# Kernel tuning notes

Measured on AMD Instinct MI355X. Metric: run time of the kernel, lower is better.

## Reference

```python
import jax, jax.numpy as jnp
import numpy as np
from jax.ops import segment_sum

N_NODES = 50000
N_EDGES = 150000
IN_FEATS = 512
OUT_FEATS = 512


def setup_inputs() -> dict:
    key = jax.random.key(0)
    k1, k2, k3, k4 = jax.random.split(key, 4)
    x = jax.random.normal(k1, (N_NODES, IN_FEATS), dtype=jnp.float32)
    src = jax.random.randint(k2, (N_EDGES,), 0, N_NODES, dtype=jnp.int64)
    dst = jax.random.randint(k3, (N_EDGES,), 0, N_NODES, dtype=jnp.int64)
    # Xavier-uniform init like reset_parameters
    limit = float(np.sqrt(6.0 / (IN_FEATS + OUT_FEATS)))
    W = jax.random.uniform(k4, (IN_FEATS, OUT_FEATS), dtype=jnp.float32,
                           minval=-limit, maxval=limit)
    b = jnp.zeros((OUT_FEATS,), dtype=jnp.float32)
    return {"x": x, "src": src, "dst": dst, "W": W, "b": b}


def reference(x, src, dst, W, b):
    # DGL GraphConv with norm='both':
    #   out = relu( D_dst^{-1/2} A D_src^{-1/2} X W + b )
    # Dropout is identity in eval mode (training=False).
    ones = jnp.ones((src.shape[0],), dtype=x.dtype)
    deg_out = segment_sum(ones, src, num_segments=N_NODES)  # source out-degree
    deg_in = segment_sum(ones, dst, num_segments=N_NODES)   # dest in-degree
    norm_src = jnp.where(deg_out > 0, deg_out, 1.0) ** -0.5  # [N]
    norm_dst = jnp.where(deg_in > 0, deg_in, 1.0) ** -0.5    # [N]

    h = x * norm_src[:, None]                         # [N, in]
    agg = segment_sum(h[src], dst, num_segments=N_NODES)  # scatter-add over edges
    agg = agg * norm_dst[:, None]                     # [N, in]
    out = agg @ W + b                                 # [N, out]
    return jax.nn.relu(out)
```

## Files before the change

### kernel.cpp

```cpp
#include <hip/hip_runtime.h>
#include <hip/hip_bf16.h>

#define N_NODES 50000
#define N_PAD   50048
#define N_EDGES 150000
#define F 512
#define BM 128
#define BN 128
#define BK 64
#define NBLK 196

typedef __attribute__((ext_vector_type(4))) float f32x4;
typedef __attribute__((ext_vector_type(4))) unsigned int u32x4;
typedef __attribute__((ext_vector_type(2))) unsigned int u32x2;

__device__ __forceinline__ unsigned short f2bf(float f) {
    unsigned int u = __float_as_uint(f);
    return (unsigned short)((u + 0x7fffu + ((u >> 16) & 1u)) >> 16);
}
__device__ __forceinline__ unsigned int pack2(float a, float b) {
    return (unsigned int)f2bf(a) | ((unsigned int)f2bf(b) << 16);
}
__device__ __forceinline__ void gload16(const void* g, void* l) {
    __builtin_amdgcn_global_load_lds(
        (const __attribute__((address_space(1))) unsigned int*)g,
        (__attribute__((address_space(3))) unsigned int*)l, 16, 0, 0);
}

__global__ void __launch_bounds__(256) crd_deg(const int* __restrict__ src,
                                               const int* __restrict__ dst,
                                               int* __restrict__ hist) {
    int e = blockIdx.x * 256 + threadIdx.x;
    if (e < N_EDGES) {
        atomicAdd(&hist[src[e]], 1);
        atomicAdd(&hist[N_NODES + dst[e]], 1);
    }
}

__global__ void __launch_bounds__(256) crd_norm(const int* __restrict__ hist,
                                                float* __restrict__ norms) {
    int i = blockIdx.x * 256 + threadIdx.x;
    if (i < 2 * N_NODES) {
        int d = hist[i];
        norms[i] = rsqrtf((float)(d > 0 ? d : 1));
    }
}

__global__ void __launch_bounds__(256) crd_bsum(const int* __restrict__ hist_in,
                                                int* __restrict__ bsum) {
    __shared__ int s[256];
    int t = threadIdx.x;
    int i = blockIdx.x * 256 + t;
    s[t] = (i < N_NODES) ? hist_in[i] : 0;
    __syncthreads();
    #pragma unroll
    for (int o = 128; o > 0; o >>= 1) {
        if (t < o) s[t] += s[t + o];
        __syncthreads();
    }
    if (t == 0) bsum[blockIdx.x] = s[0];
}

__global__ void __launch_bounds__(256) crd_bscan(const int* __restrict__ bsum,
                                                 int* __restrict__ bsumoff) {
    __shared__ int s[256];
    int t = threadIdx.x;
    int v = (t < NBLK) ? bsum[t] : 0;
    s[t] = v;
    __syncthreads();
    #pragma unroll
    for (int d = 1; d < 256; d <<= 1) {
        int add = (t >= d) ? s[t - d] : 0;
        __syncthreads();
        s[t] += add;
        __syncthreads();
    }
    if (t < NBLK) bsumoff[t] = s[t] - v;
}

__global__ void __launch_bounds__(256) crd_escan(const int* __restrict__ hist_in,
                                                 const int* __restrict__ bsumoff,
                                                 int* __restrict__ off,
                                                 int* __restrict__ cursor) {
    __shared__ int s[256];
    int t = threadIdx.x;
    int i = blockIdx.x * 256 + t;
    int v = (i < N_NODES) ? hist_in[i] : 0;
    s[t] = v;
    __syncthreads();
    #pragma unroll
    for (int d = 1; d < 256; d <<= 1) {
        int add = (t >= d) ? s[t - d] : 0;
        __syncthreads();
        s[t] += add;
        __syncthreads();
    }
    int excl = s[t] - v + bsumoff[blockIdx.x];
    if (i < N_NODES) { off[i] = excl; cursor[i] = excl; }
    if (i == N_NODES - 1) off[N_NODES] = excl + v;
}

__global__ void __launch_bounds__(256) crd_place(const int* __restrict__ src,
                                                 const int* __restrict__ dst,
                                                 int* __restrict__ cursor,
                                                 int* __restrict__ sorted) {
    int e = blockIdx.x * 256 + threadIdx.x;
    if (e < N_EDGES) {
        int slot = atomicAdd(&cursor[dst[e]], 1);
        sorted[slot] = src[e];
    }
}

__global__ void __launch_bounds__(256) crd_wt(const float* __restrict__ W,
                                              unsigned short* __restrict__ Wt) {
    int idx = blockIdx.x * 256 + threadIdx.x;
    int n = idx >> 9, k = idx & 511;
    Wt[idx] = f2bf(W[k * F + n]);
}

__global__ void __launch_bounds__(256) crd_xb(const float* __restrict__ x,
                                              unsigned short* __restrict__ xb) {
    size_t i = (size_t)(blockIdx.x * 256 + threadIdx.x) * 8;
    f32x4 v0 = *(const f32x4*)(x + i);
    f32x4 v1 = *(const f32x4*)(x + i + 4);
    u32x4 w;
    w.x = pack2(v0.x, v0.y); w.y = pack2(v0.z, v0.w);
    w.z = pack2(v1.x, v1.y); w.w = pack2(v1.z, v1.w);
    *(u32x4*)(xb + i) = w;
}

__global__ void __launch_bounds__(256) crd_gather_bf(const unsigned short* __restrict__ xb,
                                                     const int* __restrict__ sorted,
                                                     const int* __restrict__ off,
                                                     const float* __restrict__ norms,
                                                     unsigned short* __restrict__ aggb) {
    int wid = (blockIdx.x * 256 + threadIdx.x) >> 6;
    int lane = threadIdx.x & 63;
    if (wid >= N_PAD) return;
    float a0=0.f,a1=0.f,a2=0.f,a3=0.f,a4=0.f,a5=0.f,a6=0.f,a7=0.f;
    if (wid < N_NODES) {
        int e0 = off[wid], e1 = off[wid + 1];
        for (int e = e0; e < e1; ++e) {
            int s = sorted[e];
            float ns = norms[s];
            u32x4 v = *(const u32x4*)(xb + (size_t)s * F + lane * 8);
            a0 += __uint_as_float(v.x << 16) * ns;
            a1 += __uint_as_float(v.x & 0xffff0000u) * ns;
            a2 += __uint_as_float(v.y << 16) * ns;
            a3 += __uint_as_float(v.y & 0xffff0000u) * ns;
            a4 += __uint_as_float(v.z << 16) * ns;
            a5 += __uint_as_float(v.z & 0xffff0000u) * ns;
            a6 += __uint_as_float(v.w << 16) * ns;
            a7 += __uint_as_float(v.w & 0xffff0000u) * ns;
        }
        float nd = norms[N_NODES + wid];
        a0*=nd;a1*=nd;a2*=nd;a3*=nd;a4*=nd;a5*=nd;a6*=nd;a7*=nd;
    }
    u32x4 w;
    w.x = pack2(a0, a1); w.y = pack2(a2, a3);
    w.z = pack2(a4, a5); w.w = pack2(a6, a7);
    *(u32x4*)(aggb + (size_t)wid * F + lane * 8) = w;
}

__global__ void __launch_bounds__(256) crd_gather_f32(const float* __restrict__ x,
                                                      const int* __restrict__ sorted,
                                                      const int* __restrict__ off,
                                                      const float* __restrict__ norms,
                                                      unsigned short* __restrict__ aggb) {
    int wid = (blockIdx.x * 256 + threadIdx.x) >> 6;
    int lane = threadIdx.x & 63;
    if (wid >= N_PAD) return;
    f32x4 a0 = {0.f,0.f,0.f,0.f}, a1 = a0;
    if (wid < N_NODES) {
        int e0 = off[wid], e1 = off[wid + 1];
        for (int e = e0; e < e1; ++e) {
            int s = sorted[e];
            float ns = norms[s];
            const f32x4* p = (const f32x4*)(x + (size_t)s * F);
            a0 += p[lane] * ns;
            a1 += p[64 + lane] * ns;
        }
        float nd = norms[N_NODES + wid];
        a0 *= nd; a1 *= nd;
    }
    unsigned short* row = aggb + (size_t)wid * F;
    u32x2 w0, w1;
    w0.x = pack2(a0.x, a0.y); w0.y = pack2(a0.z, a0.w);
    w1.x = pack2(a1.x, a1.y); w1.y = pack2(a1.z, a1.w);
    *(u32x2*)(row + lane * 4) = w0;
    *(u32x2*)(row + 256 + lane * 4) = w1;
}

__global__ void __launch_bounds__(256, 3) crd_gemm(const unsigned short* __restrict__ aggb,
                                                   const unsigned short* __restrict__ Wt,
                                                   const float* __restrict__ bias,
                                                   float* __restrict__ out) {
    __shared__ __align__(16) unsigned short lA[8 * BM * 8];
    __shared__ __align__(16) unsigned short lB[8 * BN * 8];
    const int tid = threadIdx.x;
    const int rowbase = blockIdx.x * BM;
    const int nbase = blockIdx.y * BN;
    const int lane = tid & 63;
    const int wave = tid >> 6;
    const int wm = wave >> 1, wn = wave & 1;
    const int g = lane >> 4, r = lane & 15;

    f32x4 zero4 = {0.f, 0.f, 0.f, 0.f};
    f32x4 acc[4][4];
    #pragma unroll
    for (int i = 0; i < 4; ++i)
        #pragma unroll
        for (int j = 0; j < 4; ++j) acc[i][j] = zero4;

    for (int ks = 0; ks < F / BK; ++ks) {
        #pragma unroll
        for (int j = 0; j < 4; ++j) {
            int gg = (wave * 4 + j) * 64 + lane;
            int k8 = gg >> 7, row = gg & 127;
            gload16(aggb + (size_t)(rowbase + row) * F + ks * BK + k8 * 8,
                    &lA[(size_t)(wave * 4 + j) * 64 * 8]);
        }
        #pragma unroll
        for (int j = 0; j < 4; ++j) {
            int gg = (wave * 4 + j) * 64 + lane;
            int k8 = gg >> 7, n = gg & 127;
            gload16(Wt + (size_t)(nbase + n) * F + ks * BK + k8 * 8,
                    &lB[(size_t)(wave * 4 + j) * 64 * 8]);
        }
        __syncthreads();
        #pragma unroll
        for (int kk = 0; kk < 2; ++kk) {
            int k8 = kk * 4 + g;
            u32x4 af[4], bfr[4];
            #pragma unroll
            for (int mi = 0; mi < 4; ++mi)
                af[mi] = *(const u32x4*)&lA[(k8 * BM + wm * 64 + mi * 16 + r) * 8];
            #pragma unroll
            for (int ni = 0; ni < 4; ++ni)
                bfr[ni] = *(const u32x4*)&lB[(k8 * BN + wn * 64 + ni * 16 + r) * 8];
            #pragma unroll
            for (int mi = 0; mi < 4; ++mi)
                #pragma unroll
                for (int ni = 0; ni < 4; ++ni)
                    asm("v_mfma_f32_16x16x32_bf16 %0, %1, %2, %0"
                        : "+v"(acc[mi][ni])
                        : "v"(af[mi]), "v"(bfr[ni]));
        }
        __syncthreads();
    }
    #pragma unroll
    for (int ni = 0; ni < 4; ++ni) {
        int col = nbase + wn * 64 + ni * 16 + r;
        float bv = bias[col];
        #pragma unroll
        for (int mi = 0; mi < 4; ++mi) {
            #pragma unroll
            for (int j = 0; j < 4; ++j) {
                int row = rowbase + wm * 64 + mi * 16 + g * 4 + j;
                if (row < N_NODES) {
                    float v = acc[mi][ni][j] + bv;
                    out[(size_t)row * F + col] = v > 0.0f ? v : 0.0f;
                }
            }
        }
    }
}

extern "C" void kernel_launch(void* const* d_in, const int* in_sizes, int n_in,
                              void* d_out, int out_size, void* d_ws, size_t ws_size,
                              hipStream_t stream) {
    const float* x = (const float*)d_in[0];
    const int* src = (const int*)d_in[1];
    const int* dst = (const int*)d_in[2];
    const float* W = (const float*)d_in[3];
    const float* bias = (const float*)d_in[4];
    float* out = (float*)d_out;

    unsigned short* aggb = (unsigned short*)d_ws;
    unsigned short* Wt = aggb + (size_t)N_PAD * F;
    float* norms = (float*)(Wt + (size_t)F * F);
    int* hist = (int*)(norms + 2 * N_NODES);
    int* off = hist + 2 * N_NODES;
    int* cursor = off + N_NODES + 1;
    int* sorted = cursor + N_NODES;
    int* bsum = sorted + N_EDGES;
    int* bsumoff = bsum + NBLK;
    char* endp = (char*)(bsumoff + NBLK);
    unsigned short* xb = (unsigned short*)(((uintptr_t)endp + 63) & ~(uintptr_t)63);
    size_t need_min = (size_t)(endp - (char*)d_ws);
    size_t need_bf = (size_t)((char*)(xb + (size_t)N_NODES * F) - (char*)d_ws);
    if (ws_size < need_min) {
        hipMemsetAsync(d_out, 0, (size_t)out_size * sizeof(float), stream);
        return;
    }
    const bool use_bf = (ws_size >= need_bf);

    hipMemsetAsync(hist, 0, 2 * N_NODES * sizeof(int), stream);
    crd_deg<<<(N_EDGES + 255) / 256, 256, 0, stream>>>(src, dst, hist);
    crd_norm<<<(2 * N_NODES + 255) / 256, 256, 0, stream>>>(hist, norms);
    crd_bsum<<<NBLK, 256, 0, stream>>>(hist + N_NODES, bsum);
    crd_bscan<<<1, 256, 0, stream>>>(bsum, bsumoff);
    crd_escan<<<NBLK, 256, 0, stream>>>(hist + N_NODES, bsumoff, off, cursor);
    crd_wt<<<(F * F) / 256, 256, 0, stream>>>(W, Wt);
    crd_place<<<(N_EDGES + 255) / 256, 256, 0, stream>>>(src, dst, cursor, sorted);
    if (use_bf) {
        crd_xb<<<(int)(((size_t)N_NODES * F / 8) / 256), 256, 0, stream>>>(x, xb);
        crd_gather_bf<<<N_PAD / 4, 256, 0, stream>>>(xb, sorted, off, norms, aggb);
    } else {
        crd_gather_f32<<<N_PAD / 4, 256, 0, stream>>>(x, sorted, off, norms, aggb);
    }
    dim3 grid(N_PAD / BM, F / BN);
    crd_gemm<<<grid, 256, 0, stream>>>(aggb, Wt, bias, out);
}
```

Before: 186.1 us.

## Double-buffer GEMM LDS, swizzle blocks per XCD, prescale x and unroll gather

The GEMM now uses two LDS buffers so the next K-tile's global-to-LDS loads overlap MFMA compute. It launches a flat 1D grid with an XCD-aware swizzle so that the four N-tiles of a row block land on the same XCD and share L2. The source norm is folded into the bf16 conversion of x, and the gather is unrolled by two with separate accumulators to expose more memory-level parallelism. The cost is more LDS use and fewer waves per CU (launch bounds drop from 3 to 2), and x is rounded to bf16 after scaling rather than before.

```diff
diff --git a/kernel.cpp b/kernel.cpp
--- a/kernel.cpp
+++ b/kernel.cpp
@@ -9,6 +9,7 @@
 #define BN 128
 #define BK 64
 #define NBLK 196
+#define NWG  1564
 
 typedef __attribute__((ext_vector_type(4))) float f32x4;
 typedef __attribute__((ext_vector_type(4))) unsigned int u32x4;
@@ -119,14 +120,25 @@
 }
 
 __global__ void __launch_bounds__(256) crd_xb(const float* __restrict__ x,
+                                              const float* __restrict__ norms,
                                               unsigned short* __restrict__ xb) {
-    size_t i = (size_t)(blockIdx.x * 256 + threadIdx.x) * 8;
+    int t = blockIdx.x * 256 + threadIdx.x;
+    size_t i = (size_t)t * 8;
+    float ns = norms[t >> 6];
     f32x4 v0 = *(const f32x4*)(x + i);
     f32x4 v1 = *(const f32x4*)(x + i + 4);
+    v0 *= ns; v1 *= ns;
     u32x4 w;
     w.x = pack2(v0.x, v0.y); w.y = pack2(v0.z, v0.w);
     w.z = pack2(v1.x, v1.y); w.w = pack2(v1.z, v1.w);
     *(u32x4*)(xb + i) = w;
+}
+
+__device__ __forceinline__ void acc8(float* a, u32x4 v) {
+    a[0] += __uint_as_float(v.x << 16); a[1] += __uint_as_float(v.x & 0xffff0000u);
+    a[2] += __uint_as_float(v.y << 16); a[3] += __uint_as_float(v.y & 0xffff0000u);
+    a[4] += __uint_as_float(v.z << 16); a[5] += __uint_as_float(v.z & 0xffff0000u);
+    a[6] += __uint_as_float(v.w << 16); a[7] += __uint_as_float(v.w & 0xffff0000u);
 }
 
 __global__ void __launch_bounds__(256) crd_gather_bf(const unsigned short* __restrict__ xb,
@@ -137,28 +149,29 @@
     int wid = (blockIdx.x * 256 + threadIdx.x) >> 6;
     int lane = threadIdx.x & 63;
     if (wid >= N_PAD) return;
-    float a0=0.f,a1=0.f,a2=0.f,a3=0.f,a4=0.f,a5=0.f,a6=0.f,a7=0.f;
+    float a[8] = {0.f,0.f,0.f,0.f,0.f,0.f,0.f,0.f};
+    float b[8] = {0.f,0.f,0.f,0.f,0.f,0.f,0.f,0.f};
     if (wid < N_NODES) {
         int e0 = off[wid], e1 = off[wid + 1];
-        for (int e = e0; e < e1; ++e) {
-            int s = sorted[e];
-            float ns = norms[s];
-            u32x4 v = *(const u32x4*)(xb + (size_t)s * F + lane * 8);
-            a0 += __uint_as_float(v.x << 16) * ns;
-            a1 += __uint_as_float(v.x & 0xffff0000u) * ns;
-            a2 += __uint_as_float(v.y << 16) * ns;
-            a3 += __uint_as_float(v.y & 0xffff0000u) * ns;
-            a4 += __uint_as_float(v.z << 16) * ns;
-            a5 += __uint_as_float(v.z & 0xffff0000u) * ns;
-            a6 += __uint_as_float(v.w << 16) * ns;
-            a7 += __uint_as_float(v.w & 0xffff0000u) * ns;
+        int e = e0;
+        for (; e + 1 < e1; e += 2) {
+            int s0 = sorted[e], s1 = sorted[e + 1];
+            u32x4 v0 = *(const u32x4*)(xb + (size_t)s0 * F + lane * 8);
+            u32x4 v1 = *(const u32x4*)(xb + (size_t)s1 * F + lane * 8);
+            acc8(a, v0);
+            acc8(b, v1);
+        }
+        if (e < e1) {
+            u32x4 v0 = *(const u32x4*)(xb + (size_t)sorted[e] * F + lane * 8);
+            acc8(a, v0);
         }
         float nd = norms[N_NODES + wid];
-        a0*=nd;a1*=nd;a2*=nd;a3*=nd;a4*=nd;a5*=nd;a6*=nd;a7*=nd;
+        #pragma unroll
+        for (int j = 0; j < 8; ++j) a[j] = (a[j] + b[j]) * nd;
     }
     u32x4 w;
-    w.x = pack2(a0, a1); w.y = pack2(a2, a3);
-    w.z = pack2(a4, a5); w.w = pack2(a6, a7);
+    w.x = pack2(a[0], a[1]); w.y = pack2(a[2], a[3]);
+    w.z = pack2(a[4], a[5]); w.w = pack2(a[6], a[7]);
     *(u32x4*)(aggb + (size_t)wid * F + lane * 8) = w;
 }
 
@@ -191,15 +204,18 @@
     *(u32x2*)(row + 256 + lane * 4) = w1;
 }
 
-__global__ void __launch_bounds__(256, 3) crd_gemm(const unsigned short* __restrict__ aggb,
+__global__ void __launch_bounds__(256, 2) crd_gemm(const unsigned short* __restrict__ aggb,
                                                    const unsigned short* __restrict__ Wt,
                                                    const float* __restrict__ bias,
                                                    float* __restrict__ out) {
-    __shared__ __align__(16) unsigned short lA[8 * BM * 8];
-    __shared__ __align__(16) unsigned short lB[8 * BN * 8];
+    __shared__ __align__(16) unsigned short lA[2][8 * BM * 8];
+    __shared__ __align__(16) unsigned short lB[2][8 * BN * 8];
     const int tid = threadIdx.x;
-    const int rowbase = blockIdx.x * BM;
-    const int nbase = blockIdx.y * BN;
+    int bid = blockIdx.x;
+    int xcd = bid & 7, lid = bid >> 3;
+    int swz = (xcd < 4 ? xcd * 196 : 784 + (xcd - 4) * 195) + lid;
+    const int rowbase = (swz >> 2) * BM;
+    const int nbase = (swz & 3) * BN;
     const int lane = tid & 63;
     const int wave = tid >> 6;
     const int wm = wave >> 1, wn = wave & 1;
@@ -212,42 +228,57 @@
         #pragma unroll
         for (int j = 0; j < 4; ++j) acc[i][j] = zero4;
 
-    for (int ks = 0; ks < F / BK; ++ks) {
-        #pragma unroll
-        for (int j = 0; j < 4; ++j) {
-            int gg = (wave * 4 + j) * 64 + lane;
-            int k8 = gg >> 7, row = gg & 127;
-            gload16(aggb + (size_t)(rowbase + row) * F + ks * BK + k8 * 8,
-                    &lA[(size_t)(wave * 4 + j) * 64 * 8]);
-        }
-        #pragma unroll
-        for (int j = 0; j < 4; ++j) {
-            int gg = (wave * 4 + j) * 64 + lane;
-            int k8 = gg >> 7, n = gg & 127;
-            gload16(Wt + (size_t)(nbase + n) * F + ks * BK + k8 * 8,
-                    &lB[(size_t)(wave * 4 + j) * 64 * 8]);
-        }
-        __syncthreads();
-        #pragma unroll
-        for (int kk = 0; kk < 2; ++kk) {
-            int k8 = kk * 4 + g;
-            u32x4 af[4], bfr[4];
-            #pragma unroll
-            for (int mi = 0; mi < 4; ++mi)
-                af[mi] = *(const u32x4*)&lA[(k8 * BM + wm * 64 + mi * 16 + r) * 8];
-            #pragma unroll
-            for (int ni = 0; ni < 4; ++ni)
-                bfr[ni] = *(const u32x4*)&lB[(k8 * BN + wn * 64 + ni * 16 + r) * 8];
-            #pragma unroll
-            for (int mi = 0; mi < 4; ++mi)
-                #pragma unroll
-                for (int ni = 0; ni < 4; ++ni)
-                    asm("v_mfma_f32_16x16x32_bf16 %0, %1, %2, %0"
-                        : "+v"(acc[mi][ni])
-                        : "v"(af[mi]), "v"(bfr[ni]));
-        }
-        __syncthreads();
-    }
+#define STAGE(B, KS) do { \
+    _Pragma("unroll") \
+    for (int j_ = 0; j_ < 4; ++j_) { \
+        int gg = (wave * 4 + j_) * 64 + lane; \
+        int k8 = gg >> 7, rw = gg & 127; \
+        gload16(aggb + (size_t)(rowbase + rw) * F + (KS) * BK + k8 * 8, \
+                &lA[B][(wave * 4 + j_) * 512]); \
+    } \
+    _Pragma("unroll") \
+    for (int j_ = 0; j_ < 4; ++j_) { \
+        int gg = (wave * 4 + j_) * 64 + lane; \
+        int k8 = gg >> 7, nn = gg & 127; \
+        gload16(Wt + (size_t)(nbase + nn) * F + (KS) * BK + k8 * 8, \
+                &lB[B][(wave * 4 + j_) * 512]); \
+    } \
+} while (0)
+
+#define COMPUTE(B) do { \
+    _Pragma("unroll") \
+    for (int kk = 0; kk < 2; ++kk) { \
+        int k8 = kk * 4 + g; \
+        u32x4 af[4], bfr[4]; \
+        _Pragma("unroll") \
+        for (int mi = 0; mi < 4; ++mi) \
+            af[mi] = *(const u32x4*)&lA[B][(k8 * BM + wm * 64 + mi * 16 + r) * 8]; \
+        _Pragma("unroll") \
+        for (int ni = 0; ni < 4; ++ni) \
+            bfr[ni] = *(const u32x4*)&lB[B][(k8 * BN + wn * 64 + ni * 16 + r) * 8]; \
+        _Pragma("unroll") \
+        for (int mi = 0; mi < 4; ++mi) \
+            _Pragma("unroll") \
+            for (int ni = 0; ni < 4; ++ni) \
+                asm("v_mfma_f32_16x16x32_bf16 %0, %1, %2, %0" \
+                    : "+v"(acc[mi][ni]) : "v"(af[mi]), "v"(bfr[ni])); \
+    } \
+} while (0)
+
+    STAGE(0, 0);
+    __syncthreads();
+    #pragma unroll
+    for (int ks2 = 0; ks2 < 4; ++ks2) {
+        STAGE(1, 2 * ks2 + 1);
+        COMPUTE(0);
+        __syncthreads();
+        if (ks2 < 3) STAGE(0, 2 * ks2 + 2);
+        COMPUTE(1);
+        __syncthreads();
+    }
+#undef STAGE
+#undef COMPUTE
+
     #pragma unroll
     for (int ni = 0; ni < 4; ++ni) {
         int col = nbase + wn * 64 + ni * 16 + r;
@@ -304,11 +335,10 @@
     crd_wt<<<(F * F) / 256, 256, 0, stream>>>(W, Wt);
     crd_place<<<(N_EDGES + 255) / 256, 256, 0, stream>>>(src, dst, cursor, sorted);
     if (use_bf) {
-        crd_xb<<<(int)(((size_t)N_NODES * F / 8) / 256), 256, 0, stream>>>(x, xb);
+        crd_xb<<<(int)(((size_t)N_NODES * F / 8) / 256), 256, 0, stream>>>(x, norms, xb);
         crd_gather_bf<<<N_PAD / 4, 256, 0, stream>>>(xb, sorted, off, norms, aggb);
     } else {
         crd_gather_f32<<<N_PAD / 4, 256, 0, stream>>>(x, sorted, off, norms, aggb);
     }
-    dim3 grid(N_PAD / BM, F / BN);
-    crd_gemm<<<grid, 256, 0, stream>>>(aggb, Wt, bias, out);
-}
+    crd_gemm<<<NWG, 256, 0, stream>>>(aggb, Wt, bias, out);
+}
```

Result: slower. 196.1 us (+5.4%).
